# Kernel optimization log

Measured on AMD Instinct MI355X. Metric: run time of the kernel, lower is better.

Reference implementation:

```python
import jax, jax.numpy as jnp
import numpy as np

EPS = 1e-7            # keras.backend.epsilon()
NEG = -1e30           # log-space 'zero' (avoid -inf for NaN-free grads)
SUB_SAMPLE = (2, 2)   # encoder conv subsampling factors (non-tensor forward arg)


def setup_inputs() -> dict:
    key = jax.random.key(0)
    k1, k2, k3, k4 = jax.random.split(key, 4)
    B, T, C, L = 128, 2000, 128, 200
    logits = jax.random.normal(k1, (B, T, C), jnp.float32)
    y_pred = jax.nn.softmax(logits, axis=-1)  # ctc_batch_cost expects probabilities
    labels = jax.random.randint(k2, (B, L), 0, C - 1, jnp.int32)  # never the blank (C-1)
    # raw frame counts; after two /2 subsamplings -> in [1000, 2000] <= T
    feat_lens = jax.random.randint(k3, (B,), 4000, 8000, jnp.int32)
    label_lens = jax.random.randint(k4, (B,), 50, L + 1, jnp.int32)
    return {"y_pred": y_pred, "labels": labels, "feat_lens": feat_lens, "label_lens": label_lens}


def _ctc_batch_cost(y_pred, labels, feat_lens, label_lens):
    """Faithful reimplementation of keras.backend.ctc_batch_cost (blank = C-1),
    with the CTCLayer's subsampling of feat_lens applied first."""
    for sub in SUB_SAMPLE:
        if sub > 1:
            feat_lens = (feat_lens + 1) // sub
    log_probs = jnp.log(y_pred + EPS)                 # [B,T,C]
    B, T, C = y_pred.shape
    L = labels.shape[1]
    S = 2 * L + 1
    blank = C - 1

    # extended label sequence: blank, l1, blank, l2, ..., blank  -> [B,S]
    ext = jnp.full((B, S), blank, jnp.int32).at[:, 1::2].set(labels)
    # skip transition s-2 -> s allowed iff ext[s] != blank and ext[s] != ext[s-2]
    skip_ok = jnp.concatenate(
        [jnp.zeros((B, 2), bool), (ext[:, 2:] != blank) & (ext[:, 2:] != ext[:, :-2])],
        axis=1,
    )
    bidx = jnp.arange(B)
    i1 = 2 * label_lens - 1   # last non-blank state
    i2 = 2 * label_lens       # trailing blank state

    lp = jnp.swapaxes(log_probs, 0, 1)                # [T,B,C], scan over time

    emit0 = jnp.take_along_axis(lp[0], ext, axis=1)   # [B,S]
    alpha0 = (jnp.full((B, S), NEG, jnp.float32)
              .at[:, 0].set(emit0[:, 0])
              .at[:, 1].set(emit0[:, 1]))
    ll0 = jnp.logaddexp(alpha0[bidx, i1], alpha0[bidx, i2])
    final0 = jnp.where(feat_lens == 1, ll0, NEG)

    def step(carry, inp):
        alpha, final = carry
        t, lp_t = inp
        emit = jnp.take_along_axis(lp_t, ext, axis=1)              # [B,S]
        a1 = jnp.pad(alpha, ((0, 0), (1, 0)), constant_values=NEG)[:, :-1]
        a2 = jnp.pad(alpha, ((0, 0), (2, 0)), constant_values=NEG)[:, :-2]
        m = jnp.logaddexp(alpha, a1)
        m = jnp.where(skip_ok, jnp.logaddexp(m, a2), m)
        alpha = m + emit
        ll = jnp.logaddexp(alpha[bidx, i1], alpha[bidx, i2])
        final = jnp.where(t == feat_lens - 1, ll, final)           # capture at last valid frame
        return (alpha, final), None

    (_, final), _ = jax.lax.scan(step, (alpha0, final0), (jnp.arange(1, T), lp[1:]))
    return -final[:, None]                                          # [B,1] like ctc_batch_cost


def reference(y_pred, labels, feat_lens, label_lens):
    return _ctc_batch_cost(y_pred, labels, feat_lens, label_lens)
```

## Files before the change

kernel.cpp:

```cpp
#include <hip/hip_runtime.h>
#include <math.h>

#define EPSQ 1e-7f
#define TDIM 2000
#define CDIM 128
#define LDIM 200
#define SPL  7
#define SENTE (-(1 << 30))

#define RING  0
#define LABSI 8192
#define PRODF 8392
#define CONSF 8393
#define SMEMN 8400


__device__ __forceinline__ float dpp_shr_f(float x) {
    return __int_as_float(__builtin_amdgcn_update_dpp(0, __float_as_int(x), 0x138, 0xf, 0xf, true));
}
__device__ __forceinline__ int dpp_shr_i(int x) {
    return __builtin_amdgcn_update_dpp(0, x, 0x138, 0xf, 0xf, true);
}
__device__ __forceinline__ float dpp_shl_f(float x) {
    return __int_as_float(__builtin_amdgcn_update_dpp(0, __float_as_int(x), 0x130, 0xf, 0xf, true));
}
__device__ __forceinline__ int dpp_shl_i(int x) {
    return __builtin_amdgcn_update_dpp(0, x, 0x130, 0xf, 0xf, true);
}

__device__ __forceinline__ void renorm_alpha(float a[SPL], int& E, float& fprev, int lane) {
    float mx = fmaxf(fmaxf(fmaxf(a[0], a[1]), fmaxf(a[2], a[3])),
                     fmaxf(fmaxf(a[4], a[5]), a[6]));
    bool zero = (mx == 0.f);
    int e = ((__float_as_int(mx) >> 23) & 0xff) - 127;
    int S_self = zero ? SENTE : (E + e);
    int S1 = dpp_shr_i(S_self);
    if (lane == 0) S1 = SENTE;
    int S2 = dpp_shr_i(S1);
    if (lane == 0) S2 = SENTE;
    int E_new = max(S_self, S1);
    int E_prevnew = max(S1, S2);
    int dg = E - E_new;
    float g = (zero || dg < -126) ? 0.f : __int_as_float((dg + 127) << 23);
#pragma unroll
    for (int j = 0; j < SPL; ++j) a[j] *= g;
    E = E_new;
    int df = E_prevnew - E_new;
    bool fz = (E_prevnew <= SENTE / 2) || (df < -126);
    if (df > 126) df = 126;
    fprev = fz ? 0.f : __int_as_float((df + 127) << 23);
}

__device__ __forceinline__ void renorm_beta(float b[SPL], int& E, float& fnext, int lane) {
    float mx = fmaxf(fmaxf(fmaxf(b[0], b[1]), fmaxf(b[2], b[3])),
                     fmaxf(fmaxf(b[4], b[5]), b[6]));
    bool zero = (mx == 0.f);
    int e = ((__float_as_int(mx) >> 23) & 0xff) - 127;
    int S_self = zero ? SENTE : (E + e);
    int S1 = dpp_shl_i(S_self);
    if (lane == 63) S1 = SENTE;
    int S2 = dpp_shl_i(S1);
    if (lane == 63) S2 = SENTE;
    int E_new = max(S_self, S1);
    int E_nextnew = max(S1, S2);
    int dg = E - E_new;
    float g = (zero || dg < -126) ? 0.f : __int_as_float((dg + 127) << 23);
#pragma unroll
    for (int j = 0; j < SPL; ++j) b[j] *= g;
    E = E_new;
    int df = E_nextnew - E_new;
    bool fz = (E_nextnew <= SENTE / 2) || (df < -126);
    if (df > 126) df = 126;
    fnext = fz ? 0.f : __int_as_float((df + 127) << 23);
}

#define A_STEPF(TOFF) do {                                                    \
    float p6 = dpp_shr_f(a[6]) * fprev;                                       \
    float p5 = dpp_shr_f(a[5]) * fprev;                                       \
    float n0 = fmaf(skipf[0], p5,   a[0] + p6)   * q[(1+(TOFF))&3][0];        \
    float n1 = fmaf(skipf[1], p6,   a[1] + a[0]) * q[(1+(TOFF))&3][1];        \
    float n2 = fmaf(skipf[2], a[0], a[2] + a[1]) * q[(1+(TOFF))&3][2];        \
    float n3 = fmaf(skipf[3], a[1], a[3] + a[2]) * q[(1+(TOFF))&3][3];        \
    float n4 = fmaf(skipf[4], a[2], a[4] + a[3]) * q[(1+(TOFF))&3][4];        \
    float n5 = fmaf(skipf[5], a[3], a[5] + a[4]) * q[(1+(TOFF))&3][5];        \
    float n6 = fmaf(skipf[6], a[4], a[6] + a[5]) * q[(1+(TOFF))&3][6];        \
    a[0]=n0; a[1]=n1; a[2]=n2; a[3]=n3; a[4]=n4; a[5]=n5; a[6]=n6;            \
    _Pragma("unroll")                                                         \
    for (int j = 0; j < SPL; ++j)                                             \
        q[(TOFF)&3][j] = ring[((((TOFF)+4)&63)<<7) + cls[j]];                 \
} while (0);

#define A_TAIL(TOFF) do {                                                     \
    float p6 = dpp_shr_f(a[6]) * fprev;                                       \
    float p5 = dpp_shr_f(a[5]) * fprev;                                       \
    float n0 = fmaf(skipf[0], p5,   a[0] + p6)   * q[(1+(TOFF))&3][0];        \
    float n1 = fmaf(skipf[1], p6,   a[1] + a[0]) * q[(1+(TOFF))&3][1];        \
    float n2 = fmaf(skipf[2], a[0], a[2] + a[1]) * q[(1+(TOFF))&3][2];        \
    float n3 = fmaf(skipf[3], a[1], a[3] + a[2]) * q[(1+(TOFF))&3][3];        \
    float n4 = fmaf(skipf[4], a[2], a[4] + a[3]) * q[(1+(TOFF))&3][4];        \
    float n5 = fmaf(skipf[5], a[3], a[5] + a[4]) * q[(1+(TOFF))&3][5];        \
    float n6 = fmaf(skipf[6], a[4], a[6] + a[5]) * q[(1+(TOFF))&3][6];        \
    a[0]=n0; a[1]=n1; a[2]=n2; a[3]=n3; a[4]=n4; a[5]=n5; a[6]=n6;            \
    if (t + (TOFF) == m) {                                                    \
        _Pragma("unroll")                                                     \
        for (int j = 0; j < SPL; ++j) ac[j] = a[j];                           \
        Eac = E;                                                              \
    }                                                                         \
    {   const int rr = ((t + (TOFF) + 3) & 63) << 7;                          \
        _Pragma("unroll")                                                     \
        for (int j = 0; j < SPL; ++j)                                         \
            q[(TOFF)&3][j] = ring[rr + cls[j]];                               \
    }                                                                         \
} while (0);

#define B_STEPF(SOFF) do {                                                    \
    float c0 = bb[0]*q[(SOFF)&3][0], c1 = bb[1]*q[(SOFF)&3][1];               \
    float c2 = bb[2]*q[(SOFF)&3][2], c3 = bb[3]*q[(SOFF)&3][3];               \
    float c4 = bb[4]*q[(SOFF)&3][4], c5 = bb[5]*q[(SOFF)&3][5];               \
    float c6 = bb[6]*q[(SOFF)&3][6];                                          \
    float cn0 = dpp_shl_f(c0) * fnext;                                        \
    float cn1 = dpp_shl_f(c1) * fnext;                                        \
    bb[0] = fmaf(skb[0], c2, c0 + c1);                                        \
    bb[1] = fmaf(skb[1], c3, c1 + c2);                                        \
    bb[2] = fmaf(skb[2], c4, c2 + c3);                                        \
    bb[3] = fmaf(skb[3], c5, c3 + c4);                                        \
    bb[4] = fmaf(skb[4], c6, c4 + c5);                                        \
    bb[5] = fmaf(skb[5], cn0, c5 + c6);                                       \
    bb[6] = fmaf(skb[6], cn1, c6 + cn0);                                      \
    _Pragma("unroll")                                                         \
    for (int j = 0; j < SPL; ++j)                                             \
        q[(3+(SOFF))&3][j] = ring[((((SOFF)+3)&63)<<7) + cls[j]];             \
} while (0);

#define B_TAIL(SOFF) do {                                                     \
    float c0 = bb[0]*q[(SOFF)&3][0], c1 = bb[1]*q[(SOFF)&3][1];               \
    float c2 = bb[2]*q[(SOFF)&3][2], c3 = bb[3]*q[(SOFF)&3][3];               \
    float c4 = bb[4]*q[(SOFF)&3][4], c5 = bb[5]*q[(SOFF)&3][5];               \
    float c6 = bb[6]*q[(SOFF)&3][6];                                          \
    float cn0 = dpp_shl_f(c0) * fnext;                                        \
    float cn1 = dpp_shl_f(c1) * fnext;                                        \
    bb[0] = fmaf(skb[0], c2, c0 + c1);                                        \
    bb[1] = fmaf(skb[1], c3, c1 + c2);                                        \
    bb[2] = fmaf(skb[2], c4, c2 + c3);                                        \
    bb[3] = fmaf(skb[3], c5, c3 + c4);                                        \
    bb[4] = fmaf(skb[4], c6, c4 + c5);                                        \
    bb[5] = fmaf(skb[5], cn0, c5 + c6);                                       \
    bb[6] = fmaf(skb[6], cn1, c6 + cn0);                                      \
    if (s + (SOFF) == scap) {                                                 \
        _Pragma("unroll")                                                     \
        for (int j = 0; j < SPL; ++j) bc[j] = bb[j];                          \
        Ebc = E;                                                              \
    }                                                                         \
    {   const int rr = ((s + (SOFF) + 3) & 63) << 7;                          \
        _Pragma("unroll")                                                     \
        for (int j = 0; j < SPL; ++j)                                         \
            q[(3+(SOFF))&3][j] = ring[rr + cls[j]];                           \
    }                                                                         \
} while (0);

#define ABLK(T) renorm_alpha(a, E, fprev, lane); \
    A_STEPF(T) A_STEPF((T)+1) A_STEPF((T)+2) A_STEPF((T)+3)
#define BBLK(T) renorm_beta(bb, E, fnext, lane); \
    B_STEPF(T) B_STEPF((T)+1) B_STEPF((T)+2) B_STEPF((T)+3)

#define LOADG(W, G) do {                                                      \
    _Pragma("unroll")                                                         \
    for (int i_ = 0; i_ < 8; ++i_) {                                          \
        int ii_ = (G) * 8 + i_; if (ii_ > iend) ii_ = iend;                   \
        int pr_ = role ? (pbase - ii_) : ii_;                                 \
        W[i_] = rp4[pr_ * 64 + lane];                                         \
    }                                                                         \
} while (0)

#define STOREG(W, G) do {                                                     \
    _Pragma("unroll")                                                         \
    for (int i_ = 0; i_ < 8; ++i_) {                                          \
        int ii_ = (G) * 8 + i_; if (ii_ > iend) ii_ = iend;                   \
        int pr_ = role ? (pbase - ii_) : ii_;                                 \
        float4 x_ = W[i_];                                                    \
        x_.x += EPSQ; x_.y += EPSQ; x_.z += EPSQ; x_.w += EPSQ;               \
        int fa_;                                                              \
        if (role) { int jj_ = (Tbm1 - 2 * pr_) - (lane >> 5);                 \
                    fa_ = ((jj_ & 63) << 7) + ((lane & 31) << 2); }           \
        else      { fa_ = ((pr_ & 31) << 8) + (lane << 2); }                  \
        *(float4*)&smf[RING + fa_] = x_;                                      \
    }                                                                         \
} while (0)

__global__ void __launch_bounds__(128, 1)
__attribute__((amdgpu_waves_per_eu(1, 1)))
ctc_kernel(const float* __restrict__ y_pred,
           const int* __restrict__ labels,
           const int* __restrict__ feat_lens,
           const int* __restrict__ label_lens,
           float* __restrict__ ws)
{
    __shared__ int smem[SMEMN];
    float* smf = (float*)smem;
    volatile int* vsm = (volatile int*)smem;

    const int bid = blockIdx.x;
    const int b = bid >> 1;
    const int role = bid & 1;
    const int tid = threadIdx.x;
    const int lane = tid & 63;
    const int wv = tid >> 6;

    int f = feat_lens[b];
    f = (f + 1) >> 1; f = (f + 1) >> 1;
    const int Tbm1 = f - 1;
    const int m = f >> 1;

    if (tid < 2) smem[PRODF + tid] = 0;
    const int* labrow = labels + b * LDIM;
    for (int i = tid; i < LDIM; i += 128) smem[LABSI + i] = labrow[i];
    __syncthreads();

    const float4* rp4 = (const float4*)(y_pred + (size_t)b * TDIM * CDIM);

    if (wv == 1) {
        int iend, pbase;
        if (role == 0) { iend = (m + 18) >> 1; pbase = 0; }
        else {
            const int pstart = Tbm1 >> 1;
            int pl = (m - 18) >> 1; if (pl < 0) pl = 0;
            iend = pstart - pl; pbase = pstart;
        }
        const int ng = (iend >> 3) + 1;
        float4 w0[8], w1[8];
        LOADG(w0, 0);
        if (ng > 1) LOADG(w1, 1);
        int g = 0;
        while (true) {
            while (vsm[CONSF] + 32 < 8 * (g + 1)) __builtin_amdgcn_s_sleep(2);
            asm volatile("" ::: "memory");
            STOREG(w0, g);
            asm volatile("s_waitcnt lgkmcnt(0)" ::: "memory");
            vsm[PRODF] = 8 * (g + 1);
            if (g + 2 < ng) LOADG(w0, g + 2);
            ++g; if (g >= ng) break;
            while (vsm[CONSF] + 32 < 8 * (g + 1)) __builtin_amdgcn_s_sleep(2);
            asm volatile("" ::: "memory");
            STOREG(w1, g);
            asm volatile("s_waitcnt lgkmcnt(0)" ::: "memory");
            vsm[PRODF] = 8 * (g + 1);
            if (g + 2 < ng) LOADG(w1, g + 2);
            ++g; if (g >= ng) break;
        }
        return;
    }

    const int llen = label_lens[b];
    const int i1 = 2 * llen - 1, i2 = 2 * llen;
    int cls[SPL]; float skipf[SPL];
    const int s0 = lane * SPL;
#pragma unroll
    for (int j = 0; j < SPL; ++j) {
        int s = s0 + j;
        int c = CDIM - 1; float sk = 0.f;
        if (s < (2 * LDIM + 1) && (s & 1)) {
            int kk = s >> 1;
            c = smem[LABSI + kk];
            if (kk >= 1 && smem[LABSI + kk] != smem[LABSI + kk - 1]) sk = 1.f;
        }
        cls[j] = c; skipf[j] = sk;
    }
    const float* ring = &smf[RING];

    if (role == 0) {
        float a[SPL], q[4][SPL], ac[SPL];
        int E = 0, Eac = 0;
        float fprev = 0.f;
#pragma unroll
        for (int j = 0; j < SPL; ++j) { a[j] = 0.f; ac[j] = 0.f; }

        while (vsm[PRODF] < 2) __builtin_amdgcn_s_sleep(1);
        asm volatile("" ::: "memory");
#pragma unroll
        for (int j = 0; j < SPL; ++j) {
            q[0][j] = ring[(0 << 7) + cls[j]];
            q[1][j] = ring[(1 << 7) + cls[j]];
            q[2][j] = ring[(2 << 7) + cls[j]];
            q[3][j] = ring[(3 << 7) + cls[j]];
        }
        if (lane == 0) { a[0] = q[0][0]; a[1] = q[0][1]; }

        int t = 1;
        while (t + 64 <= m) {
            vsm[CONSF] = (t >= 2) ? (((t - 2) >> 1) + 1) : 0;
            {
                int need = ((t + 34) >> 1) + 1;
                while (vsm[PRODF] < need) __builtin_amdgcn_s_sleep(1);
                asm volatile("" ::: "memory");
            }
            ABLK(0) ABLK(4) ABLK(8) ABLK(12)
            ABLK(16) ABLK(20) ABLK(24) ABLK(28)
            {
                int tc = t + 32;
                vsm[CONSF] = ((tc - 2) >> 1) + 1;
                int need = ((tc + 34) >> 1) + 1;
                while (vsm[PRODF] < need) __builtin_amdgcn_s_sleep(1);
                asm volatile("" ::: "memory");
            }
            ABLK(32) ABLK(36) ABLK(40) ABLK(44)
            ABLK(48) ABLK(52) ABLK(56) ABLK(60)
            t += 64;
        }
        while (t <= m) {
            vsm[CONSF] = (t >= 2) ? (((t - 2) >> 1) + 1) : 0;
            int need = ((t + 18) >> 1) + 1;
            while (vsm[PRODF] < need) __builtin_amdgcn_s_sleep(1);
            asm volatile("" ::: "memory");
            renorm_alpha(a, E, fprev, lane);
            A_TAIL(0) A_TAIL(1) A_TAIL(2) A_TAIL(3)
            renorm_alpha(a, E, fprev, lane);
            A_TAIL(4) A_TAIL(5) A_TAIL(6) A_TAIL(7)
            renorm_alpha(a, E, fprev, lane);
            A_TAIL(8) A_TAIL(9) A_TAIL(10) A_TAIL(11)
            renorm_alpha(a, E, fprev, lane);
            A_TAIL(12) A_TAIL(13) A_TAIL(14) A_TAIL(15)
            t += 16;
        }
        vsm[CONSF] = 1 << 28;
        asm volatile("" ::: "memory");
        float* wsb = ws + (size_t)b * 1024;
#pragma unroll
        for (int j = 0; j < SPL; ++j) wsb[lane * SPL + j] = ac[j];
        ((int*)wsb)[448 + lane] = Eac;
    } else {
        float bb[SPL], q[4][SPL], bc[SPL];
        int E = 0, Ebc = 0;
        float fnext = 0.f;
#pragma unroll
        for (int j = 0; j < SPL; ++j) {
            int s = s0 + j;
            bb[j] = (s == i1 || s == i2) ? 1.f : 0.f;
            bc[j] = 0.f;
        }
        float skb[SPL];
#pragma unroll
        for (int j = 0; j < 5; ++j) skb[j] = skipf[j + 2];
        skb[5] = (lane == 63) ? 0.f : __shfl_down(skipf[0], 1, 64);
        skb[6] = (lane == 63) ? 0.f : __shfl_down(skipf[1], 1, 64);

        const int t0 = Tbm1;
        const int nb = t0 - m;
        const int scap = nb - 1;
        const int pstart = t0 >> 1;

        while (vsm[PRODF] < 2) __builtin_amdgcn_s_sleep(1);
        asm volatile("" ::: "memory");
#pragma unroll
        for (int j = 0; j < SPL; ++j) {
            q[0][j] = ring[(0 << 7) + cls[j]];
            q[1][j] = ring[(1 << 7) + cls[j]];
            q[2][j] = ring[(2 << 7) + cls[j]];
            q[3][j] = 0.f;
        }

        int s = 0;
        while (s + 64 <= scap) {
            {
                int tcur = t0 - s;
                vsm[CONSF] = pstart - ((tcur + 2) >> 1) + 1;
                int need = pstart - ((tcur - 34) >> 1) + 1;
                while (vsm[PRODF] < need) __builtin_amdgcn_s_sleep(1);
                asm volatile("" ::: "memory");
            }
            BBLK(0) BBLK(4) BBLK(8) BBLK(12)
            BBLK(16) BBLK(20) BBLK(24) BBLK(28)
            {
                int tcur = t0 - s - 32;
                vsm[CONSF] = pstart - ((tcur + 2) >> 1) + 1;
                int need = pstart - ((tcur - 34) >> 1) + 1;
                while (vsm[PRODF] < need) __builtin_amdgcn_s_sleep(1);
                asm volatile("" ::: "memory");
            }
            BBLK(32) BBLK(36) BBLK(40) BBLK(44)
            BBLK(48) BBLK(52) BBLK(56) BBLK(60)
            s += 64;
        }
        while (s < nb) {
            int tcur = t0 - s;
            vsm[CONSF] = pstart - ((tcur + 2) >> 1) + 1;
            int need = pstart - ((tcur - 18) >> 1) + 1;
            while (vsm[PRODF] < need) __builtin_amdgcn_s_sleep(1);
            asm volatile("" ::: "memory");
            renorm_beta(bb, E, fnext, lane);
            B_TAIL(0) B_TAIL(1) B_TAIL(2) B_TAIL(3)
            renorm_beta(bb, E, fnext, lane);
            B_TAIL(4) B_TAIL(5) B_TAIL(6) B_TAIL(7)
            renorm_beta(bb, E, fnext, lane);
            B_TAIL(8) B_TAIL(9) B_TAIL(10) B_TAIL(11)
            renorm_beta(bb, E, fnext, lane);
            B_TAIL(12) B_TAIL(13) B_TAIL(14) B_TAIL(15)
            s += 16;
        }
        vsm[CONSF] = 1 << 28;
        asm volatile("" ::: "memory");
        float* wsb = ws + (size_t)b * 1024 + 512;
#pragma unroll
        for (int j = 0; j < SPL; ++j) wsb[lane * SPL + j] = bc[j];
        ((int*)wsb)[448 + lane] = Ebc;
    }
}

__global__ void __launch_bounds__(64, 1)
ctc_combine(const float* __restrict__ ws, float* __restrict__ out)
{
    const int b = blockIdx.x;
    const int lane = threadIdx.x & 63;
    const float* wa = ws + (size_t)b * 1024;
    const float* wb = wa + 512;
    const int Ea = ((const int*)wa)[448 + lane];
    const int Eb = ((const int*)wb)[448 + lane];
    float dot = 0.f;
#pragma unroll
    for (int j = 0; j < SPL; ++j)
        dot = fmaf(wa[lane * SPL + j], wb[lane * SPL + j], dot);
    float l2 = (dot > 0.f) ? (log2f(dot) + (float)(Ea + Eb)) : -1e30f;
    float M = l2;
#pragma unroll
    for (int d = 1; d < 64; d <<= 1) M = fmaxf(M, __shfl_xor(M, d, 64));
    float S = exp2f(l2 - M);
#pragma unroll
    for (int d = 1; d < 64; d <<= 1) S += __shfl_xor(S, d, 64);
    if (lane == 0) out[b] = -(M + log2f(S)) * 0.69314718055994530942f;
}

extern "C" void kernel_launch(void* const* d_in, const int* in_sizes, int n_in,
                              void* d_out, int out_size, void* d_ws, size_t ws_size,
                              hipStream_t stream) {
    (void)n_in; (void)out_size; (void)ws_size;
    const float* y_pred     = (const float*)d_in[0];
    const int*   labels     = (const int*)d_in[1];
    const int*   feat_lens  = (const int*)d_in[2];
    const int*   label_lens = (const int*)d_in[3];
    float* out = (float*)d_out;
    float* ws  = (float*)d_ws;
    const int B = in_sizes[2];
    ctc_kernel<<<B * 2, 128, 0, stream>>>(y_pred, labels, feat_lens, label_lens, ws);
    ctc_combine<<<B, 64, 0, stream>>>(ws, out);
}
```

Before: 250.4 us.

## Pre-gather emission probabilities per lane into vectorized LDS array with two producer waves

Producer waves now do the per-state class gather from the raw LDS staging buffer themselves. They write a per-lane contiguous array of the 7 emission values (two float4 per step), so the compute wave issues two 16-byte LDS loads per timestep instead of seven scattered scalar loads. Producer work is split across two waves (block grows from 128 to 192 threads) with separate progress flags, and the consumer waits on both. This takes LDS gather latency off the serial recurrence critical path. In exchange it uses much more shared memory, adds extra LDS traffic and a third wave, and makes producer/consumer synchronization more complex.

```diff
diff --git a/kernel.cpp b/kernel.cpp
--- a/kernel.cpp
+++ b/kernel.cpp
@@ -8,12 +8,12 @@
 #define SPL  7
 #define SENTE (-(1 << 30))
 
-#define RING  0
-#define LABSI 8192
-#define PRODF 8392
-#define CONSF 8393
-#define SMEMN 8400
-
+#define LABSI 2048
+#define PRODF1 2248
+#define PRODF2 2249
+#define CONSF 2250
+#define ARRB  9216
+#define SMEMN 35072
 
 __device__ __forceinline__ float dpp_shr_f(float x) {
     return __int_as_float(__builtin_amdgcn_update_dpp(0, __float_as_int(x), 0x138, 0xf, 0xf, true));
@@ -74,50 +74,54 @@
     fnext = fz ? 0.f : __int_as_float((df + 127) << 23);
 }
 
+#define ARD(X) (*(const float4*)((((X) < 65536) ? arC : arC2) + ((X) & 65535)))
+
+#define APB(TOFF) (((((TOFF)+4)&63))<<11)
 #define A_STEPF(TOFF) do {                                                    \
     float p6 = dpp_shr_f(a[6]) * fprev;                                       \
     float p5 = dpp_shr_f(a[5]) * fprev;                                       \
-    float n0 = fmaf(skipf[0], p5,   a[0] + p6)   * q[(1+(TOFF))&3][0];        \
-    float n1 = fmaf(skipf[1], p6,   a[1] + a[0]) * q[(1+(TOFF))&3][1];        \
-    float n2 = fmaf(skipf[2], a[0], a[2] + a[1]) * q[(1+(TOFF))&3][2];        \
-    float n3 = fmaf(skipf[3], a[1], a[3] + a[2]) * q[(1+(TOFF))&3][3];        \
-    float n4 = fmaf(skipf[4], a[2], a[4] + a[3]) * q[(1+(TOFF))&3][4];        \
-    float n5 = fmaf(skipf[5], a[3], a[5] + a[4]) * q[(1+(TOFF))&3][5];        \
-    float n6 = fmaf(skipf[6], a[4], a[6] + a[5]) * q[(1+(TOFF))&3][6];        \
+    float4 qa = qA[(1+(TOFF))&3], qb = qB[(1+(TOFF))&3];                      \
+    float n0 = fmaf(skipf[0], p5,   a[0] + p6)   * qa.x;                      \
+    float n1 = fmaf(skipf[1], p6,   a[1] + a[0]) * qa.y;                      \
+    float n2 = fmaf(skipf[2], a[0], a[2] + a[1]) * qa.z;                      \
+    float n3 = fmaf(skipf[3], a[1], a[3] + a[2]) * qa.w;                      \
+    float n4 = fmaf(skipf[4], a[2], a[4] + a[3]) * qb.x;                      \
+    float n5 = fmaf(skipf[5], a[3], a[5] + a[4]) * qb.y;                      \
+    float n6 = fmaf(skipf[6], a[4], a[6] + a[5]) * qb.z;                      \
     a[0]=n0; a[1]=n1; a[2]=n2; a[3]=n3; a[4]=n4; a[5]=n5; a[6]=n6;            \
-    _Pragma("unroll")                                                         \
-    for (int j = 0; j < SPL; ++j)                                             \
-        q[(TOFF)&3][j] = ring[((((TOFF)+4)&63)<<7) + cls[j]];                 \
+    qA[(TOFF)&3] = ARD(APB(TOFF));                                            \
+    qB[(TOFF)&3] = ARD(APB(TOFF)+1024);                                       \
 } while (0);
 
 #define A_TAIL(TOFF) do {                                                     \
     float p6 = dpp_shr_f(a[6]) * fprev;                                       \
     float p5 = dpp_shr_f(a[5]) * fprev;                                       \
-    float n0 = fmaf(skipf[0], p5,   a[0] + p6)   * q[(1+(TOFF))&3][0];        \
-    float n1 = fmaf(skipf[1], p6,   a[1] + a[0]) * q[(1+(TOFF))&3][1];        \
-    float n2 = fmaf(skipf[2], a[0], a[2] + a[1]) * q[(1+(TOFF))&3][2];        \
-    float n3 = fmaf(skipf[3], a[1], a[3] + a[2]) * q[(1+(TOFF))&3][3];        \
-    float n4 = fmaf(skipf[4], a[2], a[4] + a[3]) * q[(1+(TOFF))&3][4];        \
-    float n5 = fmaf(skipf[5], a[3], a[5] + a[4]) * q[(1+(TOFF))&3][5];        \
-    float n6 = fmaf(skipf[6], a[4], a[6] + a[5]) * q[(1+(TOFF))&3][6];        \
+    float4 qa = qA[(1+(TOFF))&3], qb = qB[(1+(TOFF))&3];                      \
+    float n0 = fmaf(skipf[0], p5,   a[0] + p6)   * qa.x;                      \
+    float n1 = fmaf(skipf[1], p6,   a[1] + a[0]) * qa.y;                      \
+    float n2 = fmaf(skipf[2], a[0], a[2] + a[1]) * qa.z;                      \
+    float n3 = fmaf(skipf[3], a[1], a[3] + a[2]) * qa.w;                      \
+    float n4 = fmaf(skipf[4], a[2], a[4] + a[3]) * qb.x;                      \
+    float n5 = fmaf(skipf[5], a[3], a[5] + a[4]) * qb.y;                      \
+    float n6 = fmaf(skipf[6], a[4], a[6] + a[5]) * qb.z;                      \
     a[0]=n0; a[1]=n1; a[2]=n2; a[3]=n3; a[4]=n4; a[5]=n5; a[6]=n6;            \
     if (t + (TOFF) == m) {                                                    \
         _Pragma("unroll")                                                     \
         for (int j = 0; j < SPL; ++j) ac[j] = a[j];                           \
         Eac = E;                                                              \
     }                                                                         \
-    {   const int rr = ((t + (TOFF) + 3) & 63) << 7;                          \
-        _Pragma("unroll")                                                     \
-        for (int j = 0; j < SPL; ++j)                                         \
-            q[(TOFF)&3][j] = ring[rr + cls[j]];                               \
-    }                                                                         \
+    {   int ro_ = ((t + (TOFF) + 3) & 63) << 11;                              \
+        qA[(TOFF)&3] = *(const float4*)(arC + ro_);                           \
+        qB[(TOFF)&3] = *(const float4*)(arC + ro_ + 1024); }                  \
 } while (0);
 
+#define BPB(SOFF) (((((SOFF)+3)&63))<<11)
 #define B_STEPF(SOFF) do {                                                    \
-    float c0 = bb[0]*q[(SOFF)&3][0], c1 = bb[1]*q[(SOFF)&3][1];               \
-    float c2 = bb[2]*q[(SOFF)&3][2], c3 = bb[3]*q[(SOFF)&3][3];               \
-    float c4 = bb[4]*q[(SOFF)&3][4], c5 = bb[5]*q[(SOFF)&3][5];               \
-    float c6 = bb[6]*q[(SOFF)&3][6];                                          \
+    float4 qa = qA[(SOFF)&3], qb = qB[(SOFF)&3];                              \
+    float c0 = bb[0]*qa.x, c1 = bb[1]*qa.y;                                   \
+    float c2 = bb[2]*qa.z, c3 = bb[3]*qa.w;                                   \
+    float c4 = bb[4]*qb.x, c5 = bb[5]*qb.y;                                   \
+    float c6 = bb[6]*qb.z;                                                    \
     float cn0 = dpp_shl_f(c0) * fnext;                                        \
     float cn1 = dpp_shl_f(c1) * fnext;                                        \
     bb[0] = fmaf(skb[0], c2, c0 + c1);                                        \
@@ -127,16 +131,16 @@
     bb[4] = fmaf(skb[4], c6, c4 + c5);                                        \
     bb[5] = fmaf(skb[5], cn0, c5 + c6);                                       \
     bb[6] = fmaf(skb[6], cn1, c6 + cn0);                                      \
-    _Pragma("unroll")                                                         \
-    for (int j = 0; j < SPL; ++j)                                             \
-        q[(3+(SOFF))&3][j] = ring[((((SOFF)+3)&63)<<7) + cls[j]];             \
+    qA[(3+(SOFF))&3] = ARD(BPB(SOFF));                                        \
+    qB[(3+(SOFF))&3] = ARD(BPB(SOFF)+1024);                                   \
 } while (0);
 
 #define B_TAIL(SOFF) do {                                                     \
-    float c0 = bb[0]*q[(SOFF)&3][0], c1 = bb[1]*q[(SOFF)&3][1];               \
-    float c2 = bb[2]*q[(SOFF)&3][2], c3 = bb[3]*q[(SOFF)&3][3];               \
-    float c4 = bb[4]*q[(SOFF)&3][4], c5 = bb[5]*q[(SOFF)&3][5];               \
-    float c6 = bb[6]*q[(SOFF)&3][6];                                          \
+    float4 qa = qA[(SOFF)&3], qb = qB[(SOFF)&3];                              \
+    float c0 = bb[0]*qa.x, c1 = bb[1]*qa.y;                                   \
+    float c2 = bb[2]*qa.z, c3 = bb[3]*qa.w;                                   \
+    float c4 = bb[4]*qb.x, c5 = bb[5]*qb.y;                                   \
+    float c6 = bb[6]*qb.z;                                                    \
     float cn0 = dpp_shl_f(c0) * fnext;                                        \
     float cn1 = dpp_shl_f(c1) * fnext;                                        \
     bb[0] = fmaf(skb[0], c2, c0 + c1);                                        \
@@ -151,11 +155,9 @@
         for (int j = 0; j < SPL; ++j) bc[j] = bb[j];                          \
         Ebc = E;                                                              \
     }                                                                         \
-    {   const int rr = ((s + (SOFF) + 3) & 63) << 7;                          \
-        _Pragma("unroll")                                                     \
-        for (int j = 0; j < SPL; ++j)                                         \
-            q[(3+(SOFF))&3][j] = ring[rr + cls[j]];                           \
-    }                                                                         \
+    {   int ro_ = ((s + (SOFF) + 3) & 63) << 11;                              \
+        qA[(3+(SOFF))&3] = *(const float4*)(arC + ro_);                       \
+        qB[(3+(SOFF))&3] = *(const float4*)(arC + ro_ + 1024); }              \
 } while (0);
 
 #define ABLK(T) renorm_alpha(a, E, fprev, lane); \
@@ -163,31 +165,59 @@
 #define BBLK(T) renorm_beta(bb, E, fnext, lane); \
     B_STEPF(T) B_STEPF((T)+1) B_STEPF((T)+2) B_STEPF((T)+3)
 
+#define WAITP(NEED) do { int nd_ = (NEED);                                    \
+    while (vsm[PRODF1] < nd_ || vsm[PRODF2] < nd_)                            \
+        __builtin_amdgcn_s_sleep(1);                                          \
+    asm volatile("" ::: "memory"); } while (0)
+
 #define LOADG(W, G) do {                                                      \
     _Pragma("unroll")                                                         \
-    for (int i_ = 0; i_ < 8; ++i_) {                                          \
-        int ii_ = (G) * 8 + i_; if (ii_ > iend) ii_ = iend;                   \
+    for (int k_ = 0; k_ < 4; ++k_) {                                          \
+        int ii_ = (G) * 8 + P4 + k_; if (ii_ > iend) ii_ = iend;              \
         int pr_ = role ? (pbase - ii_) : ii_;                                 \
-        W[i_] = rp4[pr_ * 64 + lane];                                         \
+        W[k_] = rp4[pr_ * 64 + lane];                                         \
     }                                                                         \
 } while (0)
 
-#define STOREG(W, G) do {                                                     \
+#define STORERAW(W) do {                                                      \
     _Pragma("unroll")                                                         \
-    for (int i_ = 0; i_ < 8; ++i_) {                                          \
-        int ii_ = (G) * 8 + i_; if (ii_ > iend) ii_ = iend;                   \
-        int pr_ = role ? (pbase - ii_) : ii_;                                 \
-        float4 x_ = W[i_];                                                    \
+    for (int k_ = 0; k_ < 4; ++k_) {                                          \
+        float4 x_ = W[k_];                                                    \
         x_.x += EPSQ; x_.y += EPSQ; x_.z += EPSQ; x_.w += EPSQ;               \
-        int fa_;                                                              \
-        if (role) { int jj_ = (Tbm1 - 2 * pr_) - (lane >> 5);                 \
-                    fa_ = ((jj_ & 63) << 7) + ((lane & 31) << 2); }           \
-        else      { fa_ = ((pr_ & 31) << 8) + (lane << 2); }                  \
-        *(float4*)&smf[RING + fa_] = x_;                                      \
+        *(float4*)(rawWB + k_ * 1024 + (lane << 4)) = x_;                     \
     }                                                                         \
 } while (0)
 
-__global__ void __launch_bounds__(128, 1)
+#define GATH(RI, A, B) do {                                                   \
+    A.x = rdF[((RI) << 7) + cls[0]]; A.y = rdF[((RI) << 7) + cls[1]];         \
+    A.z = rdF[((RI) << 7) + cls[2]]; A.w = rdF[((RI) << 7) + cls[3]];         \
+    B.x = rdF[((RI) << 7) + cls[4]]; B.y = rdF[((RI) << 7) + cls[5]];         \
+    B.z = rdF[((RI) << 7) + cls[6]]; B.w = B.z;                               \
+} while (0)
+
+#define WRARR(R, A, B) do {                                                   \
+    int pi_ = g8 + P4 + ((R) >> 1); if (pi_ > iend) pi_ = iend;               \
+    int pr_ = role ? (pbase - pi_) : pi_;                                     \
+    int row_ = 2 * pr_ + ((R) & 1);                                           \
+    if (!role || row_ <= Tbm1) {                                              \
+        int sl_ = role ? ((Tbm1 - row_) & 63) : (row_ & 63);                  \
+        char* d_ = arrWB + (sl_ << 11) + (lane << 4);                         \
+        *(float4*)d_ = A; *(float4*)(d_ + 1024) = B;                          \
+    }                                                                         \
+} while (0)
+
+#define PGROUP(G) do { int g8 = 8 * (G);                                      \
+    GATH(0, A0, B0); GATH(1, A1, B1);                                         \
+    WRARR(0, A0, B0); GATH(2, A0, B0);                                        \
+    WRARR(1, A1, B1); GATH(3, A1, B1);                                        \
+    WRARR(2, A0, B0); GATH(4, A0, B0);                                        \
+    WRARR(3, A1, B1); GATH(5, A1, B1);                                        \
+    WRARR(4, A0, B0); GATH(6, A0, B0);                                        \
+    WRARR(5, A1, B1); GATH(7, A1, B1);                                        \
+    WRARR(6, A0, B0); WRARR(7, A1, B1);                                       \
+} while (0)
+
+__global__ void __launch_bounds__(192, 1)
 __attribute__((amdgpu_waves_per_eu(1, 1)))
 ctc_kernel(const float* __restrict__ y_pred,
            const int* __restrict__ labels,
@@ -211,47 +241,11 @@
     const int Tbm1 = f - 1;
     const int m = f >> 1;
 
-    if (tid < 2) smem[PRODF + tid] = 0;
+    if (tid < 3) smem[PRODF1 + tid] = 0;
     const int* labrow = labels + b * LDIM;
-    for (int i = tid; i < LDIM; i += 128) smem[LABSI + i] = labrow[i];
+    for (int i = tid; i < LDIM; i += 192) smem[LABSI + i] = labrow[i];
     __syncthreads();
 
-    const float4* rp4 = (const float4*)(y_pred + (size_t)b * TDIM * CDIM);
-
-    if (wv == 1) {
-        int iend, pbase;
-        if (role == 0) { iend = (m + 18) >> 1; pbase = 0; }
-        else {
-            const int pstart = Tbm1 >> 1;
-            int pl = (m - 18) >> 1; if (pl < 0) pl = 0;
-            iend = pstart - pl; pbase = pstart;
-        }
-        const int ng = (iend >> 3) + 1;
-        float4 w0[8], w1[8];
-        LOADG(w0, 0);
-        if (ng > 1) LOADG(w1, 1);
-        int g = 0;
-        while (true) {
-            while (vsm[CONSF] + 32 < 8 * (g + 1)) __builtin_amdgcn_s_sleep(2);
-            asm volatile("" ::: "memory");
-            STOREG(w0, g);
-            asm volatile("s_waitcnt lgkmcnt(0)" ::: "memory");
-            vsm[PRODF] = 8 * (g + 1);
-            if (g + 2 < ng) LOADG(w0, g + 2);
-            ++g; if (g >= ng) break;
-            while (vsm[CONSF] + 32 < 8 * (g + 1)) __builtin_amdgcn_s_sleep(2);
-            asm volatile("" ::: "memory");
-            STOREG(w1, g);
-            asm volatile("s_waitcnt lgkmcnt(0)" ::: "memory");
-            vsm[PRODF] = 8 * (g + 1);
-            if (g + 2 < ng) LOADG(w1, g + 2);
-            ++g; if (g >= ng) break;
-        }
-        return;
-    }
-
-    const int llen = label_lens[b];
-    const int i1 = 2 * llen - 1, i2 = 2 * llen;
     int cls[SPL]; float skipf[SPL];
     const int s0 = lane * SPL;
 #pragma unroll
@@ -265,42 +259,81 @@
         }
         cls[j] = c; skipf[j] = sk;
     }
-    const float* ring = &smf[RING];
+
+    const float4* rp4 = (const float4*)(y_pred + (size_t)b * TDIM * CDIM);
+
+    if (wv != 0) {
+        const int P4 = (wv - 1) * 4;
+        char* rawWB = (char*)smem + (P4 << 10);
+        const float* rdF = smf + (P4 << 8);
+        char* arrWB = (char*)smem + ARRB;
+        int iend, pbase;
+        if (role == 0) { iend = (m + 18) >> 1; pbase = 0; }
+        else {
+            const int pstart = Tbm1 >> 1;
+            int pl = (m - 18) >> 1; if (pl < 0) pl = 0;
+            iend = pstart - pl; pbase = pstart;
+        }
+        const int ng = (iend >> 3) + 1;
+        const int PF = (wv == 1) ? PRODF1 : PRODF2;
+        float4 w0[4], w1[4];
+        float4 A0, B0, A1, B1;
+        LOADG(w0, 0);
+        if (ng > 1) LOADG(w1, 1);
+        int g = 0;
+        while (true) {
+            while (vsm[CONSF] + 32 < 8 * (g + 1)) __builtin_amdgcn_s_sleep(2);
+            asm volatile("" ::: "memory");
+            STORERAW(w0);
+            asm volatile("s_waitcnt lgkmcnt(0)" ::: "memory");
+            PGROUP(g);
+            asm volatile("s_waitcnt lgkmcnt(0)" ::: "memory");
+            vsm[PF] = 8 * (g + 1);
+            if (g + 2 < ng) LOADG(w0, g + 2);
+            ++g; if (g >= ng) break;
+            while (vsm[CONSF] + 32 < 8 * (g + 1)) __builtin_amdgcn_s_sleep(2);
+            asm volatile("" ::: "memory");
+            STORERAW(w1);
+            asm volatile("s_waitcnt lgkmcnt(0)" ::: "memory");
+            PGROUP(g);
+            asm volatile("s_waitcnt lgkmcnt(0)" ::: "memory");
+            vsm[PF] = 8 * (g + 1);
+            if (g + 2 < ng) LOADG(w1, g + 2);
+            ++g; if (g >= ng) break;
+        }
+        return;
+    }
+
+    const char* arC  = (const char*)smem + ARRB + (lane << 4);
+    const char* arC2 = arC + 65536;
+    const int llen = label_lens[b];
+    const int i1 = 2 * llen - 1, i2 = 2 * llen;
 
     if (role == 0) {
-        float a[SPL], q[4][SPL], ac[SPL];
+        float a[SPL], ac[SPL];
+        float4 qA[4], qB[4];
         int E = 0, Eac = 0;
         float fprev = 0.f;
 #pragma unroll
         for (int j = 0; j < SPL; ++j) { a[j] = 0.f; ac[j] = 0.f; }
 
-        while (vsm[PRODF] < 2) __builtin_amdgcn_s_sleep(1);
-        asm volatile("" ::: "memory");
-#pragma unroll
-        for (int j = 0; j < SPL; ++j) {
-            q[0][j] = ring[(0 << 7) + cls[j]];
-            q[1][j] = ring[(1 << 7) + cls[j]];
-            q[2][j] = ring[(2 << 7) + cls[j]];
-            q[3][j] = ring[(3 << 7) + cls[j]];
-        }
-        if (lane == 0) { a[0] = q[0][0]; a[1] = q[0][1]; }
+        WAITP(2);
+        qA[0] = ARD(0);    qB[0] = ARD(1024);
+        qA[1] = ARD(2048); qB[1] = ARD(2048+1024);
+        qA[2] = ARD(4096); qB[2] = ARD(4096+1024);
+        qA[3] = ARD(6144); qB[3] = ARD(6144+1024);
+        if (lane == 0) { a[0] = qA[0].x; a[1] = qA[0].y; }
 
         int t = 1;
         while (t + 64 <= m) {
             vsm[CONSF] = (t >= 2) ? (((t - 2) >> 1) + 1) : 0;
-            {
-                int need = ((t + 34) >> 1) + 1;
-                while (vsm[PRODF] < need) __builtin_amdgcn_s_sleep(1);
-                asm volatile("" ::: "memory");
-            }
+            WAITP(((t + 34) >> 1) + 1);
             ABLK(0) ABLK(4) ABLK(8) ABLK(12)
             ABLK(16) ABLK(20) ABLK(24) ABLK(28)
             {
                 int tc = t + 32;
                 vsm[CONSF] = ((tc - 2) >> 1) + 1;
-                int need = ((tc + 34) >> 1) + 1;
-                while (vsm[PRODF] < need) __builtin_amdgcn_s_sleep(1);
-                asm volatile("" ::: "memory");
+                WAITP(((tc + 34) >> 1) + 1);
             }
             ABLK(32) ABLK(36) ABLK(40) ABLK(44)
             ABLK(48) ABLK(52) ABLK(56) ABLK(60)
@@ -308,9 +341,7 @@
         }
         while (t <= m) {
             vsm[CONSF] = (t >= 2) ? (((t - 2) >> 1) + 1) : 0;
-            int need = ((t + 18) >> 1) + 1;
-            while (vsm[PRODF] < need) __builtin_amdgcn_s_sleep(1);
-            asm volatile("" ::: "memory");
+            WAITP(((t + 18) >> 1) + 1);
             renorm_alpha(a, E, fprev, lane);
             A_TAIL(0) A_TAIL(1) A_TAIL(2) A_TAIL(3)
             renorm_alpha(a, E, fprev, lane);
@@ -328,7 +359,8 @@
         for (int j = 0; j < SPL; ++j) wsb[lane * SPL + j] = ac[j];
         ((int*)wsb)[448 + lane] = Eac;
     } else {
-        float bb[SPL], q[4][SPL], bc[SPL];
+        float bb[SPL], bc[SPL];
+        float4 qA[4], qB[4];
         int E = 0, Ebc = 0;
         float fnext = 0.f;
 #pragma unroll
@@ -348,33 +380,25 @@
         const int scap = nb - 1;
         const int pstart = t0 >> 1;
 
-        while (vsm[PRODF] < 2) __builtin_amdgcn_s_sleep(1);
-        asm volatile("" ::: "memory");
-#pragma unroll
-        for (int j = 0; j < SPL; ++j) {
-            q[0][j] = ring[(0 << 7) + cls[j]];
-            q[1][j] = ring[(1 << 7) + cls[j]];
-            q[2][j] = ring[(2 << 7) + cls[j]];
-            q[3][j] = 0.f;
-        }
+        WAITP(2);
+        qA[0] = ARD(0);    qB[0] = ARD(1024);
+        qA[1] = ARD(2048); qB[1] = ARD(2048+1024);
+        qA[2] = ARD(4096); qB[2] = ARD(4096+1024);
+        qA[3] = make_float4(0.f,0.f,0.f,0.f); qB[3] = qA[3];
 
         int s = 0;
         while (s + 64 <= scap) {
             {
                 int tcur = t0 - s;
                 vsm[CONSF] = pstart - ((tcur + 2) >> 1) + 1;
-                int need = pstart - ((tcur - 34) >> 1) + 1;
-                while (vsm[PRODF] < need) __builtin_amdgcn_s_sleep(1);
-                asm volatile("" ::: "memory");
+                WAITP(pstart - ((tcur - 34) >> 1) + 1);
             }
             BBLK(0) BBLK(4) BBLK(8) BBLK(12)
             BBLK(16) BBLK(20) BBLK(24) BBLK(28)
             {
                 int tcur = t0 - s - 32;
                 vsm[CONSF] = pstart - ((tcur + 2) >> 1) + 1;
-                int need = pstart - ((tcur - 34) >> 1) + 1;
-                while (vsm[PRODF] < need) __builtin_amdgcn_s_sleep(1);
-                asm volatile("" ::: "memory");
+                WAITP(pstart - ((tcur - 34) >> 1) + 1);
             }
             BBLK(32) BBLK(36) BBLK(40) BBLK(44)
             BBLK(48) BBLK(52) BBLK(56) BBLK(60)
@@ -383,9 +407,7 @@
         while (s < nb) {
             int tcur = t0 - s;
             vsm[CONSF] = pstart - ((tcur + 2) >> 1) + 1;
-            int need = pstart - ((tcur - 18) >> 1) + 1;
-            while (vsm[PRODF] < need) __builtin_amdgcn_s_sleep(1);
-            asm volatile("" ::: "memory");
+            WAITP(pstart - ((tcur - 18) >> 1) + 1);
             renorm_beta(bb, E, fnext, lane);
             B_TAIL(0) B_TAIL(1) B_TAIL(2) B_TAIL(3)
             renorm_beta(bb, E, fnext, lane);
@@ -439,6 +461,6 @@
     float* out = (float*)d_out;
     float* ws  = (float*)d_ws;
     const int B = in_sizes[2];
-    ctc_kernel<<<B * 2, 128, 0, stream>>>(y_pred, labels, feat_lens, label_lens, ws);
+    ctc_kernel<<<B * 2, 192, 0, stream>>>(y_pred, labels, feat_lens, label_lens, ws);
     ctc_combine<<<B, 64, 0, stream>>>(ws, out);
 }
```

Result: slower. 267.2 us (+6.7%).
